# Kernel tuning notes

Hardware: AMD Instinct MI355X
Metric: run time of the kernel (lower is better)

Reference implementation:

```python
import jax, jax.numpy as jnp
import numpy as np

C = 1024
HEADS = 8
HD = C // HEADS
SF = 2
EPS = 1e-6
N, D, H, W = 2, 32, 40, 32


def _ln(x, w, b):
    m = jnp.mean(x, -1, keepdims=True)
    v = jnp.mean((x - m) ** 2, -1, keepdims=True)
    return (x - m) * jax.lax.rsqrt(v + EPS) * w + b


def _mlp2(x, w1, b1, w2, b2):
    # Linear -> exact GELU -> Linear (matches nn.Sequential(Linear, GELU, Linear))
    return jax.nn.gelu(x @ w1.T + b1, approximate=False) @ w2.T + b2


def setup_inputs() -> dict:
    key = jax.random.key(0)
    ks = jax.random.split(key, 24)
    p = lambda i, shape: jax.random.normal(ks[i], shape, jnp.float32) * 0.02
    return {
        "x": jax.random.normal(ks[0], (N, D, H, W, C), jnp.float32),
        "q_w": p(1, (C, C)),
        "k_w1": p(2, (C, C)), "k_b1": p(3, (C,)),
        "k_w2": p(4, (C, C)), "k_b2": p(5, (C,)),
        "v_w1": p(6, (C, C)), "v_b1": p(7, (C,)),
        "v_w2": p(8, (C, C)), "v_b2": p(9, (C,)),
        "lnq_w": jnp.ones((C,), jnp.float32), "lnq_b": jnp.zeros((C,), jnp.float32),
        "lnk_w": jnp.ones((C,), jnp.float32), "lnk_b": jnp.zeros((C,), jnp.float32),
        "lnv_w": jnp.ones((C,), jnp.float32), "lnv_b": jnp.zeros((C,), jnp.float32),
        "in_w": p(10, (3 * C, C)), "in_b": p(11, (3 * C,)),
        "out_w": p(12, (C, C)), "out_b": p(13, (C,)),
        "mlp_w1": p(14, (2 * C, C)), "mlp_b1": p(15, (2 * C,)),
        "mlp_w2": p(16, (2 * C, 2 * C)), "mlp_b2": p(17, (2 * C,)),
    }


def reference(x, q_w, k_w1, k_b1, k_w2, k_b2, v_w1, v_b1, v_w2, v_b2,
              lnq_w, lnq_b, lnk_w, lnk_b, lnv_w, lnv_b,
              in_w, in_b, out_w, out_b, mlp_w1, mlp_b1, mlp_w2, mlp_b2):
    n, d, h, w, c = x.shape
    dg, hg, wg = d // SF, h // SF, w // SF
    cube = SF ** 3

    x_flat = x.reshape(n, -1, c)                      # [N, T, C], T = D*H*W
    k = _ln(_mlp2(x_flat, k_w1, k_b1, k_w2, k_b2), lnk_w, lnk_b)
    v = _ln(_mlp2(x_flat, v_w1, v_b1, v_w2, v_b2), lnv_w, lnv_b)

    # Trilinear downsample by exactly 2 (align_corners=False) == 2x2x2 mean pool.
    q = x.reshape(n, dg, SF, hg, SF, wg, SF, c).mean(axis=(2, 4, 6))
    q = q.reshape(n, -1, c)                            # [N, Q, C]
    query = _ln(q @ q_w.T, lnq_w, lnq_b)               # q_proj_1 has no bias

    def regions(t):
        t = t.reshape(n, dg, SF, hg, SF, wg, SF, c)
        t = t.transpose(0, 1, 3, 5, 2, 4, 6, 7)
        return t.reshape(n, dg * hg * wg, cube, c)     # [N, Q, 8, C]

    k_r = regions(k)
    v_r = regions(v)

    wq, wk, wv = in_w[:C], in_w[C:2 * C], in_w[2 * C:]
    bq, bk, bv = in_b[:C], in_b[C:2 * C], in_b[2 * C:]
    qh = (query @ wq.T + bq).reshape(n, -1, HEADS, HD)           # [N,Q,h,hd]
    kh = (k_r @ wk.T + bk).reshape(n, -1, cube, HEADS, HD)       # [N,Q,8,h,hd]
    vh = (v_r @ wv.T + bv).reshape(n, -1, cube, HEADS, HD)

    scale = 1.0 / np.sqrt(HD).astype(np.float32)
    scores = jnp.einsum('nqhd,nqkhd->nqhk', qh, kh) * scale
    attn = jax.nn.softmax(scores, axis=-1)
    o = jnp.einsum('nqhk,nqkhd->nqhd', attn, vh).reshape(n, -1, c)
    o = o @ out_w.T + out_b                            # MHA out_proj

    o = _mlp2(o, mlp_w1, mlp_b1, mlp_w2, mlp_b2)       # [N, Q, 2C]
    return o.reshape(n, dg, hg, wg, 2 * c)
```

## Files before the change

kernel.cpp:

```cpp
#include <hip/hip_runtime.h>

typedef __attribute__((ext_vector_type(8))) short bf16x8;
typedef __attribute__((ext_vector_type(4))) float f32x4;
typedef unsigned short u16;

__device__ inline u16 f2b(float f) {
  union { float f; unsigned u; } x; x.f = f;
  unsigned r = x.u + 0x7FFFu + ((x.u >> 16) & 1u);
  return (u16)(r >> 16);
}
__device__ inline float b2f(u16 s) {
  union { unsigned u; float f; } x; x.u = ((unsigned)s) << 16;
  return x.f;
}
__device__ inline float gelu_f(float v) {
  return 0.5f * v * (1.0f + erff(v * 0.70710678118654752f));
}
__device__ inline void gll16(const void* g, void* lds) {
  __builtin_amdgcn_global_load_lds((const __attribute__((address_space(1))) void*)g,
                                   (__attribute__((address_space(3))) void*)lds,
                                   16, 0, 0);
}

__global__ __launch_bounds__(256) void cvt_w(const float* __restrict__ s,
                                             u16* __restrict__ d, int n4) {
  int i = blockIdx.x * 256 + threadIdx.x;
  if (i < n4) {
    float4 v = ((const float4*)s)[i];
    ushort4 o; o.x = f2b(v.x); o.y = f2b(v.y); o.z = f2b(v.z); o.w = f2b(v.w);
    ((ushort4*)d)[i] = o;
  }
}

__global__ __launch_bounds__(256) void cat_bias(const float* __restrict__ a,
                                                const float* __restrict__ b,
                                                float* __restrict__ o) {
  int i = blockIdx.x * 256 + threadIdx.x;
  if (i < 1024) { o[i] = a[i]; o[1024 + i] = b[i]; }
}

__global__ __launch_bounds__(256) void pool_cvt(const float* __restrict__ xg,
                                                u16* __restrict__ Xb,
                                                u16* __restrict__ Qp) {
  int qr = blockIdx.x;
  int wgi = qr & 15;
  int hgi = (qr >> 4) % 20;
  int dgi = qr / 320;
  int c = threadIdx.x * 4;
  float sx = 0.f, sy = 0.f, sz = 0.f, sw = 0.f;
#pragma unroll
  for (int j = 0; j < 8; ++j) {
    int tr = ((2 * dgi + (j >> 2)) * 40 + (2 * hgi + ((j >> 1) & 1))) * 32 +
             (2 * wgi + (j & 1));
    long off = (long)tr * 1024 + c;
    float4 v = *(const float4*)&xg[off];
    ushort4 o; o.x = f2b(v.x); o.y = f2b(v.y); o.z = f2b(v.z); o.w = f2b(v.w);
    *(ushort4*)&Xb[off] = o;
    sx += v.x; sy += v.y; sz += v.z; sw += v.w;
  }
  ushort4 o;
  o.x = f2b(sx * 0.125f); o.y = f2b(sy * 0.125f);
  o.z = f2b(sz * 0.125f); o.w = f2b(sw * 0.125f);
  *(ushort4*)&Qp[(long)qr * 1024 + c] = o;
}

__global__ __launch_bounds__(256) void ln_ip(u16* __restrict__ X,
                                             const float* __restrict__ w,
                                             const float* __restrict__ b) {
  long row = blockIdx.x;
  int c = threadIdx.x * 4;
  ushort4 v = *(const ushort4*)&X[row * 1024 + c];
  float f0 = b2f(v.x), f1 = b2f(v.y), f2 = b2f(v.z), f3 = b2f(v.w);
  float s = f0 + f1 + f2 + f3;
  float q = f0 * f0 + f1 * f1 + f2 * f2 + f3 * f3;
#pragma unroll
  for (int off = 32; off >= 1; off >>= 1) {
    s += __shfl_xor(s, off);
    q += __shfl_xor(q, off);
  }
  __shared__ float red[8];
  int wv = threadIdx.x >> 6, ln = threadIdx.x & 63;
  if (ln == 0) { red[wv] = s; red[4 + wv] = q; }
  __syncthreads();
  s = red[0] + red[1] + red[2] + red[3];
  q = red[4] + red[5] + red[6] + red[7];
  float mean = s * (1.f / 1024.f);
  float var = q * (1.f / 1024.f) - mean * mean;
  float rs = rsqrtf(var + 1e-6f);
  float4 wv4 = *(const float4*)&w[c];
  float4 bv4 = *(const float4*)&b[c];
  ushort4 o;
  o.x = f2b((f0 - mean) * rs * wv4.x + bv4.x);
  o.y = f2b((f1 - mean) * rs * wv4.y + bv4.y);
  o.z = f2b((f2 - mean) * rs * wv4.z + bv4.z);
  o.w = f2b((f3 - mean) * rs * wv4.w + bv4.w);
  *(ushort4*)&X[row * 1024 + c] = o;
}

#define BK 32
template <int EPI>
__global__ __launch_bounds__(256) void gemm_bt(const u16* __restrict__ A,
                                               const u16* __restrict__ B,
                                               const float* __restrict__ bias,
                                               float* __restrict__ Cf,
                                               u16* __restrict__ Cb,
                                               int M, int N, int K, int lda,
                                               int nbx, int nby) {
  __shared__ __align__(16) u16 As0[128 * BK];
  __shared__ __align__(16) u16 Bs0[128 * BK];
  __shared__ __align__(16) u16 As1[128 * BK];
  __shared__ __align__(16) u16 Bs1[128 * BK];
  const int tid = threadIdx.x;

  int L = blockIdx.x, bx, by;
  if ((nbx & 7) == 0) {
    int xcd = L & 7, j = L >> 3, ppx = nbx >> 3;
    int pj = j / nby;
    bx = xcd * ppx + pj;
    by = j - pj * nby;
  } else {
    bx = L % nbx;
    by = L / nbx;
  }
  const int bm = bx * 128, bn = by * 128;

  const int l = tid & 63, wv = tid >> 6;
  const int wm = (wv >> 1) * 64, wn = (wv & 1) * 64;
  const int lr = l & 15, kg = l >> 4;

  const int ea = tid * 8, eb = (256 + tid) * 8;
  const int ra = ea >> 5, ca = ea & 31;
  const int rb = eb >> 5, cbn = eb & 31;
  int gra = bm + ra; if (gra > M - 1) gra = M - 1;
  int grb = bm + rb; if (grb > M - 1) grb = M - 1;
  const u16* pa0 = A + (long)gra * lda + ca;
  const u16* pa1 = A + (long)grb * lda + cbn;
  const u16* pb0 = B + (long)(bn + ra) * K + ca;
  const u16* pb1 = B + (long)(bn + rb) * K + cbn;

  f32x4 acc[4][4] = {};
  const int nt = K / BK;

#define STAGE(AS, BS, k0)                \
  do {                                   \
    gll16(pa0 + (k0), &(AS)[ea]);        \
    gll16(pb0 + (k0), &(BS)[ea]);        \
    gll16(pa1 + (k0), &(AS)[eb]);        \
    gll16(pb1 + (k0), &(BS)[eb]);        \
  } while (0)

#define COMPUTE(AS, BS)                                                       \
  do {                                                                        \
    bf16x8 af[4], bfr[4];                                                     \
    _Pragma("unroll") for (int m = 0; m < 4; ++m)                             \
        af[m] = *(const bf16x8*)&(AS)[(wm + m * 16 + lr) * BK + kg * 8];      \
    _Pragma("unroll") for (int n = 0; n < 4; ++n)                             \
        bfr[n] = *(const bf16x8*)&(BS)[(wn + n * 16 + lr) * BK + kg * 8];     \
    _Pragma("unroll") for (int m = 0; m < 4; ++m)                             \
        _Pragma("unroll") for (int n = 0; n < 4; ++n)                         \
            acc[m][n] = __builtin_amdgcn_mfma_f32_16x16x32_bf16(              \
                af[m], bfr[n], acc[m][n], 0, 0, 0);                           \
  } while (0)

  STAGE(As0, Bs0, 0);
  __syncthreads();
  for (int t = 0; t < nt; t += 2) {
    if (t + 1 < nt) STAGE(As1, Bs1, (t + 1) * BK);
    COMPUTE(As0, Bs0);
    __syncthreads();
    if (t + 2 < nt) STAGE(As0, Bs0, (t + 2) * BK);
    COMPUTE(As1, Bs1);
    __syncthreads();
  }
#undef STAGE
#undef COMPUTE

#pragma unroll
  for (int m = 0; m < 4; ++m) {
    int row0 = bm + wm + m * 16 + kg * 4;
#pragma unroll
    for (int n = 0; n < 4; ++n) {
      int col = bn + wn + n * 16 + lr;
      float bsv = (EPI == 3) ? 0.f : bias[col];
#pragma unroll
      for (int r = 0; r < 4; ++r) {
        int row = row0 + r;
        if (row < M) {
          float v = acc[m][n][r] + bsv;
          if (EPI == 1) v = gelu_f(v);
          if (EPI == 2) Cf[(long)row * N + col] = v;
          else Cb[(long)row * N + col] = f2b(v);
        }
      }
    }
  }
}

__global__ __launch_bounds__(256) void attn_k(const u16* __restrict__ QH,
                                              const u16* __restrict__ KH,
                                              const u16* __restrict__ VH,
                                              u16* __restrict__ O) {
  int qr = blockIdx.x;
  int wgi = qr & 15;
  int hgi = (qr >> 4) % 20;
  int dgi = qr / 320;
  int c0 = (threadIdx.x >> 5) * 128 + (threadIdx.x & 31) * 4;
  ushort4 qv = *(const ushort4*)&QH[(long)qr * 1024 + c0];
  float q0 = b2f(qv.x), q1 = b2f(qv.y), q2 = b2f(qv.z), q3 = b2f(qv.w);
  long trs[8];
  float sc[8];
#pragma unroll
  for (int j = 0; j < 8; ++j) {
    int tr = ((2 * dgi + (j >> 2)) * 40 + (2 * hgi + ((j >> 1) & 1))) * 32 +
             (2 * wgi + (j & 1));
    trs[j] = (long)tr * 1024 + c0;
    ushort4 kv = *(const ushort4*)&KH[trs[j]];
    float p = q0 * b2f(kv.x) + q1 * b2f(kv.y) + q2 * b2f(kv.z) + q3 * b2f(kv.w);
    p += __shfl_xor(p, 16); p += __shfl_xor(p, 8); p += __shfl_xor(p, 4);
    p += __shfl_xor(p, 2);  p += __shfl_xor(p, 1);
    sc[j] = p * 0.088388347648318447f;
  }
  float mx = sc[0];
#pragma unroll
  for (int j = 1; j < 8; ++j) mx = fmaxf(mx, sc[j]);
  float ssum = 0.f;
#pragma unroll
  for (int j = 0; j < 8; ++j) { sc[j] = expf(sc[j] - mx); ssum += sc[j]; }
  float inv = 1.0f / ssum;
  float o0 = 0, o1 = 0, o2 = 0, o3 = 0;
#pragma unroll
  for (int j = 0; j < 8; ++j) {
    ushort4 vv = *(const ushort4*)&VH[trs[j]];
    float p = sc[j] * inv;
    o0 += p * b2f(vv.x); o1 += p * b2f(vv.y);
    o2 += p * b2f(vv.z); o3 += p * b2f(vv.w);
  }
  ushort4 ov; ov.x = f2b(o0); ov.y = f2b(o1); ov.z = f2b(o2); ov.w = f2b(o3);
  *(ushort4*)&O[(long)qr * 1024 + c0] = ov;
}

extern "C" void kernel_launch(void* const* d_in, const int* in_sizes, int n_in,
                              void* d_out, int out_size, void* d_ws,
                              size_t ws_size, hipStream_t stream) {
  const float* x      = (const float*)d_in[0];
  const float* q_w    = (const float*)d_in[1];
  const float* k_w1   = (const float*)d_in[2];
  const float* k_b1   = (const float*)d_in[3];
  const float* k_w2   = (const float*)d_in[4];
  const float* k_b2   = (const float*)d_in[5];
  const float* v_w1   = (const float*)d_in[6];
  const float* v_b1   = (const float*)d_in[7];
  const float* v_w2   = (const float*)d_in[8];
  const float* v_b2   = (const float*)d_in[9];
  const float* lnq_w  = (const float*)d_in[10];
  const float* lnq_b  = (const float*)d_in[11];
  const float* lnk_w  = (const float*)d_in[12];
  const float* lnk_b  = (const float*)d_in[13];
  const float* lnv_w  = (const float*)d_in[14];
  const float* lnv_b  = (const float*)d_in[15];
  const float* in_w   = (const float*)d_in[16];
  const float* in_b   = (const float*)d_in[17];
  const float* out_w  = (const float*)d_in[18];
  const float* out_b  = (const float*)d_in[19];
  const float* mlp_w1 = (const float*)d_in[20];
  const float* mlp_b1 = (const float*)d_in[21];
  const float* mlp_w2 = (const float*)d_in[22];
  const float* mlp_b2 = (const float*)d_in[23];
  float* out = (float*)d_out;

  char* base = (char*)d_ws;
  size_t off = 0;
  auto alloc_us = [&](size_t elems) -> u16* {
    u16* r = (u16*)(base + off);
    off += ((elems * 2 + 255) & ~(size_t)255);
    return r;
  };
  const size_t CC = 1024 * 1024;
  u16* wb_q   = alloc_us(CC);
  u16* wb_kv1 = alloc_us(2 * CC);
  u16* wb_k2  = alloc_us(CC);
  u16* wb_v2  = alloc_us(CC);
  u16* wb_in  = alloc_us(3 * CC);
  u16* wb_out = alloc_us(CC);
  u16* wb_m1  = alloc_us(2 * CC);
  u16* wb_m2  = alloc_us(4 * CC);
  float* b_kv1 = (float*)(base + off); off += 2048 * 4;

  auto cvt = [&](const float* s, u16* d, size_t n) {
    int n4 = (int)(n / 4);
    cvt_w<<<(n4 + 255) / 256, 256, 0, stream>>>(s, d, n4);
  };
  cvt(q_w, wb_q, CC);
  cvt(k_w1, wb_kv1, CC);        cvt(v_w1, wb_kv1 + CC, CC);
  cvt(k_w2, wb_k2, CC);         cvt(v_w2, wb_v2, CC);
  cvt(in_w, wb_in, 3 * CC);     cvt(out_w, wb_out, CC);
  cvt(mlp_w1, wb_m1, 2 * CC);   cvt(mlp_w2, wb_m2, 4 * CC);
  cat_bias<<<4, 256, 0, stream>>>(k_b1, v_b1, b_kv1);

  int s = 16;
  for (int cand = 1; cand <= 16; cand <<= 1) {
    size_t Tc_ = 40960ull / cand;
    size_t need = off + Tc_ * 11520ull + (1ull << 20);
    if (need <= ws_size) { s = cand; break; }
  }
  const int dcount = 32 / s;
  const int dgc = dcount / 2;
  const int Tc = dcount * 1280;
  const int Tq = dgc * 320;

  u16* Xb  = alloc_us((size_t)Tc * 1024);
  u16* Hb2 = alloc_us((size_t)Tc * 2048);
  u16* Kb  = alloc_us((size_t)Tc * 1024);
  u16* Vb  = alloc_us((size_t)Tc * 1024);
  u16* Qp  = alloc_us((size_t)Tq * 1024);
  u16* QQ  = alloc_us((size_t)Tq * 1024);
  u16* QHb = alloc_us((size_t)Tq * 1024);
  u16* Ob  = alloc_us((size_t)Tq * 1024);
  u16* O2  = alloc_us((size_t)Tq * 1024);
  u16* Hm  = Kb;

  auto launch_gemm = [&](int EPI, const u16* A, const u16* B, const float* bias,
                         float* Cf, u16* Cb, int M, int N, int K, int lda) {
    int nbx = (M + 127) / 128, nby = N / 128;
    dim3 g(nbx * nby);
    switch (EPI) {
      case 0: gemm_bt<0><<<g, 256, 0, stream>>>(A, B, bias, Cf, Cb, M, N, K, lda, nbx, nby); break;
      case 1: gemm_bt<1><<<g, 256, 0, stream>>>(A, B, bias, Cf, Cb, M, N, K, lda, nbx, nby); break;
      case 2: gemm_bt<2><<<g, 256, 0, stream>>>(A, B, bias, Cf, Cb, M, N, K, lda, nbx, nby); break;
      default: gemm_bt<3><<<g, 256, 0, stream>>>(A, B, bias, Cf, Cb, M, N, K, lda, nbx, nby); break;
    }
  };

  for (int n = 0; n < 2; ++n) {
    for (int sl = 0; sl < s; ++sl) {
      long tok0 = (long)n * 40960 + (long)sl * dcount * 1280;
      long q0g  = (long)n * 5120 + (long)sl * dgc * 320;
      const float* xg = x + tok0 * 1024;

      pool_cvt<<<Tq, 256, 0, stream>>>(xg, Xb, Qp);

      launch_gemm(1, Xb, wb_kv1, b_kv1, nullptr, Hb2, Tc, 2048, 1024, 1024);
      launch_gemm(0, Hb2, wb_k2, k_b2, nullptr, Kb, Tc, 1024, 1024, 2048);
      ln_ip<<<Tc, 256, 0, stream>>>(Kb, lnk_w, lnk_b);
      launch_gemm(0, Hb2 + 1024, wb_v2, v_b2, nullptr, Vb, Tc, 1024, 1024, 2048);
      ln_ip<<<Tc, 256, 0, stream>>>(Vb, lnv_w, lnv_b);

      launch_gemm(3, Qp, wb_q, nullptr, nullptr, QQ, Tq, 1024, 1024, 1024);
      ln_ip<<<Tq, 256, 0, stream>>>(QQ, lnq_w, lnq_b);
      launch_gemm(0, QQ, wb_in, in_b, nullptr, QHb, Tq, 1024, 1024, 1024);

      launch_gemm(0, Kb, wb_in + CC, in_b + 1024, nullptr, Xb, Tc, 1024, 1024, 1024);
      launch_gemm(0, Vb, wb_in + 2 * CC, in_b + 2048, nullptr, Hb2, Tc, 1024, 1024, 1024);

      attn_k<<<Tq, 256, 0, stream>>>(QHb, Xb, Hb2, Ob);

      launch_gemm(0, Ob, wb_out, out_b, nullptr, O2, Tq, 1024, 1024, 1024);
      launch_gemm(1, O2, wb_m1, mlp_b1, nullptr, Hm, Tq, 2048, 1024, 1024);
      launch_gemm(2, Hm, wb_m2, mlp_b2, out + q0g * 2048, nullptr, Tq, 2048, 2048, 2048);
    }
  }
}
```

Measured before the change: 2.314 ms.

## Replace 128x128 GEMM with 256x256 tile, 8-wave, swizzled LDS pipelined kernel

Replaces the 128x128x32 double-buffered GEMM with a 256x256x64 kernel that runs 8 waves per block and uses 128 KB of dynamic LDS. LDS rows are XOR-swizzled to avoid bank conflicts, and global-to-LDS loads are split into half-tiles interleaved between four MFMA phases. Those phases use s_setprio and explicit vmcnt waits to overlap memory with compute. The goal is more operand reuse per tile and less load latency. The cost is fewer blocks in flight, wasted work on partial tiles, and heavy register pressure from a 32-accumulator tile per wave.

```diff
diff --git a/kernel.cpp b/kernel.cpp
--- a/kernel.cpp
+++ b/kernel.cpp
@@ -97,20 +97,25 @@
   *(ushort4*)&X[row * 1024 + c] = o;
 }
 
-#define BK 32
+#define HALF 8192
+#define MFMA16(a, b, c) __builtin_amdgcn_mfma_f32_16x16x32_bf16((a), (b), (c), 0, 0, 0)
+
 template <int EPI>
-__global__ __launch_bounds__(256) void gemm_bt(const u16* __restrict__ A,
-                                               const u16* __restrict__ B,
-                                               const float* __restrict__ bias,
-                                               float* __restrict__ Cf,
-                                               u16* __restrict__ Cb,
-                                               int M, int N, int K, int lda,
-                                               int nbx, int nby) {
-  __shared__ __align__(16) u16 As0[128 * BK];
-  __shared__ __align__(16) u16 Bs0[128 * BK];
-  __shared__ __align__(16) u16 As1[128 * BK];
-  __shared__ __align__(16) u16 Bs1[128 * BK];
+__global__ __launch_bounds__(512, 2) void gemm256(const u16* __restrict__ A,
+                                                  const u16* __restrict__ B,
+                                                  const float* __restrict__ bias,
+                                                  float* __restrict__ Cf,
+                                                  u16* __restrict__ Cb,
+                                                  int M, int N, int K, int lda,
+                                                  int nbx, int nby) {
+  extern __shared__ u16 lds[];
+  u16* ASm = lds;
+  u16* BSm = lds + 4 * HALF;
   const int tid = threadIdx.x;
+  const int l = tid & 63, w = tid >> 6;
+  const int wr = w >> 2, wc = w & 3;
+  const int lr = l & 15, kg = l >> 4;
+  const int e7 = l & 7;
 
   int L = blockIdx.x, bx, by;
   if ((nbx & 7) == 0) {
@@ -122,74 +127,145 @@
     bx = L % nbx;
     by = L / nbx;
   }
-  const int bm = bx * 128, bn = by * 128;
-
-  const int l = tid & 63, wv = tid >> 6;
-  const int wm = (wv >> 1) * 64, wn = (wv & 1) * 64;
-  const int lr = l & 15, kg = l >> 4;
-
-  const int ea = tid * 8, eb = (256 + tid) * 8;
-  const int ra = ea >> 5, ca = ea & 31;
-  const int rb = eb >> 5, cbn = eb & 31;
-  int gra = bm + ra; if (gra > M - 1) gra = M - 1;
-  int grb = bm + rb; if (grb > M - 1) grb = M - 1;
-  const u16* pa0 = A + (long)gra * lda + ca;
-  const u16* pa1 = A + (long)grb * lda + cbn;
-  const u16* pb0 = B + (long)(bn + ra) * K + ca;
-  const u16* pb1 = B + (long)(bn + rb) * K + cbn;
-
-  f32x4 acc[4][4] = {};
-  const int nt = K / BK;
-
-#define STAGE(AS, BS, k0)                \
-  do {                                   \
-    gll16(pa0 + (k0), &(AS)[ea]);        \
-    gll16(pb0 + (k0), &(BS)[ea]);        \
-    gll16(pa1 + (k0), &(AS)[eb]);        \
-    gll16(pb1 + (k0), &(BS)[eb]);        \
-  } while (0)
-
-#define COMPUTE(AS, BS)                                                       \
-  do {                                                                        \
-    bf16x8 af[4], bfr[4];                                                     \
-    _Pragma("unroll") for (int m = 0; m < 4; ++m)                             \
-        af[m] = *(const bf16x8*)&(AS)[(wm + m * 16 + lr) * BK + kg * 8];      \
-    _Pragma("unroll") for (int n = 0; n < 4; ++n)                             \
-        bfr[n] = *(const bf16x8*)&(BS)[(wn + n * 16 + lr) * BK + kg * 8];     \
-    _Pragma("unroll") for (int m = 0; m < 4; ++m)                             \
-        _Pragma("unroll") for (int n = 0; n < 4; ++n)                         \
-            acc[m][n] = __builtin_amdgcn_mfma_f32_16x16x32_bf16(              \
-                af[m], bfr[n], acc[m][n], 0, 0, 0);                           \
-  } while (0)
-
-  STAGE(As0, Bs0, 0);
-  __syncthreads();
-  for (int t = 0; t < nt; t += 2) {
-    if (t + 1 < nt) STAGE(As1, Bs1, (t + 1) * BK);
-    COMPUTE(As0, Bs0);
-    __syncthreads();
-    if (t + 2 < nt) STAGE(As0, Bs0, (t + 2) * BK);
-    COMPUTE(As1, Bs1);
-    __syncthreads();
-  }
-#undef STAGE
-#undef COMPUTE
-
-#pragma unroll
-  for (int m = 0; m < 4; ++m) {
-    int row0 = bm + wm + m * 16 + kg * 4;
+  const int bm = bx * 256, bn = by * 256;
+
+  const int c0 = w * 64 + l, c1 = 512 + c0;
+  const int r0 = c0 >> 3, cs0 = (c0 & 7) ^ (r0 & 7);
+  const int r1 = c1 >> 3, cs1 = (c1 & 7) ^ (r1 & 7);
+  const u16* Ab = A + (long)bm * lda;
+  const u16* Bb = B + (long)bn * K;
+  int a0r0 = min(bm + r0, M - 1) - bm;
+  int a0r1 = min(bm + r1, M - 1) - bm;
+  int a1r0 = min(bm + 128 + r0, M - 1) - bm;
+  int a1r1 = min(bm + 128 + r1, M - 1) - bm;
+  const int oA00 = a0r0 * lda + cs0 * 8, oA01 = a0r1 * lda + cs1 * 8;
+  const int oA10 = a1r0 * lda + cs0 * 8, oA11 = a1r1 * lda + cs1 * 8;
+  const int oB00 = r0 * K + cs0 * 8, oB01 = r1 * K + cs1 * 8;
+  const int oB10 = (128 + r0) * K + cs0 * 8, oB11 = (128 + r1) * K + cs1 * 8;
+  const int d0 = c0 * 8, d1 = c1 * 8;
+
+  const int sw0 = ((kg) ^ e7) * 8;
+  const int sw1 = ((4 + kg) ^ e7) * 8;
+
+  f32x4 acc[8][4] = {};
+  bf16x8 af[4][2], bf[2][2][2];
+  const int nt = K / 64;
+
+#define STG_A(slot, o0_, o1_, ko) do { \
+    gll16(Ab + (o0_) + (ko), ASm + (slot) * HALF + d0); \
+    gll16(Ab + (o1_) + (ko), ASm + (slot) * HALF + d1); } while (0)
+#define STG_B(slot, o0_, o1_, ko) do { \
+    gll16(Bb + (o0_) + (ko), BSm + (slot) * HALF + d0); \
+    gll16(Bb + (o1_) + (ko), BSm + (slot) * HALF + d1); } while (0)
+
+  STG_A(0, oA00, oA01, 0); STG_A(1, oA10, oA11, 0);
+  STG_B(0, oB00, oB01, 0); STG_B(1, oB10, oB11, 0);
+  STG_A(2, oA00, oA01, 64); STG_B(2, oB00, oB01, 64); STG_B(3, oB10, oB11, 64);
+  asm volatile("s_waitcnt vmcnt(6)" ::: "memory");
+  __builtin_amdgcn_s_barrier();
+
+  const int rbA = wr * 64 + lr;
+  const int rbB = (wc & 1) * 64 + lr;
+
+  for (int t = 0; t < nt; ++t) {
+    const int p = t & 1, qp = p ^ 1;
+    const int kn1 = (t + 1 < nt ? t + 1 : nt - 1) * 64;
+    const int kn2 = (t + 2 < nt ? t + 2 : nt - 1) * 64;
+    const u16* sa0 = ASm + (p * 2 + 0) * HALF;
+    const u16* sa1 = ASm + (p * 2 + 1) * HALF;
+    const u16* sb = BSm + (p * 2 + (wc >> 1)) * HALF;
+
+#pragma unroll
+    for (int mq = 0; mq < 4; ++mq) {
+      af[mq][0] = *(const bf16x8*)&sa0[(rbA + mq * 16) * 64 + sw0];
+      af[mq][1] = *(const bf16x8*)&sa0[(rbA + mq * 16) * 64 + sw1];
+    }
+#pragma unroll
+    for (int nn = 0; nn < 2; ++nn) {
+      bf[0][nn][0] = *(const bf16x8*)&sb[(rbB + nn * 16) * 64 + sw0];
+      bf[0][nn][1] = *(const bf16x8*)&sb[(rbB + nn * 16) * 64 + sw1];
+    }
+    STG_A(qp * 2 + 1, oA10, oA11, kn1);
+    __builtin_amdgcn_s_barrier();
+    __builtin_amdgcn_s_setprio(1);
+#pragma unroll
+    for (int mq = 0; mq < 4; ++mq)
+#pragma unroll
+      for (int nn = 0; nn < 2; ++nn) {
+        acc[mq][nn] = MFMA16(af[mq][0], bf[0][nn][0], acc[mq][nn]);
+        acc[mq][nn] = MFMA16(af[mq][1], bf[0][nn][1], acc[mq][nn]);
+      }
+    __builtin_amdgcn_s_setprio(0);
+    __builtin_amdgcn_s_barrier();
+
+#pragma unroll
+    for (int nn = 0; nn < 2; ++nn) {
+      bf[1][nn][0] = *(const bf16x8*)&sb[(rbB + (2 + nn) * 16) * 64 + sw0];
+      bf[1][nn][1] = *(const bf16x8*)&sb[(rbB + (2 + nn) * 16) * 64 + sw1];
+    }
+    STG_A(p * 2 + 0, oA00, oA01, kn2);
+    __builtin_amdgcn_s_barrier();
+    __builtin_amdgcn_s_setprio(1);
+#pragma unroll
+    for (int mq = 0; mq < 4; ++mq)
+#pragma unroll
+      for (int nn = 0; nn < 2; ++nn) {
+        acc[mq][2 + nn] = MFMA16(af[mq][0], bf[1][nn][0], acc[mq][2 + nn]);
+        acc[mq][2 + nn] = MFMA16(af[mq][1], bf[1][nn][1], acc[mq][2 + nn]);
+      }
+    __builtin_amdgcn_s_setprio(0);
+    __builtin_amdgcn_s_barrier();
+
+#pragma unroll
+    for (int mq = 0; mq < 4; ++mq) {
+      af[mq][0] = *(const bf16x8*)&sa1[(rbA + mq * 16) * 64 + sw0];
+      af[mq][1] = *(const bf16x8*)&sa1[(rbA + mq * 16) * 64 + sw1];
+    }
+    STG_B(p * 2 + 0, oB00, oB01, kn2);
+    __builtin_amdgcn_s_barrier();
+    __builtin_amdgcn_s_setprio(1);
+#pragma unroll
+    for (int mq = 0; mq < 4; ++mq)
+#pragma unroll
+      for (int nn = 0; nn < 2; ++nn) {
+        acc[4 + mq][nn] = MFMA16(af[mq][0], bf[0][nn][0], acc[4 + mq][nn]);
+        acc[4 + mq][nn] = MFMA16(af[mq][1], bf[0][nn][1], acc[4 + mq][nn]);
+      }
+    __builtin_amdgcn_s_setprio(0);
+    __builtin_amdgcn_s_barrier();
+
+    STG_B(p * 2 + 1, oB10, oB11, kn2);
+    asm volatile("s_waitcnt vmcnt(6)" ::: "memory");
+    __builtin_amdgcn_s_barrier();
+    __builtin_amdgcn_s_setprio(1);
+#pragma unroll
+    for (int mq = 0; mq < 4; ++mq)
+#pragma unroll
+      for (int nn = 0; nn < 2; ++nn) {
+        acc[4 + mq][2 + nn] = MFMA16(af[mq][0], bf[1][nn][0], acc[4 + mq][2 + nn]);
+        acc[4 + mq][2 + nn] = MFMA16(af[mq][1], bf[1][nn][1], acc[4 + mq][2 + nn]);
+      }
+    __builtin_amdgcn_s_setprio(0);
+    __builtin_amdgcn_s_barrier();
+  }
+  asm volatile("s_waitcnt vmcnt(0)" ::: "memory");
+#undef STG_A
+#undef STG_B
+
+#pragma unroll
+  for (int m = 0; m < 8; ++m) {
+    int row = bm + (m >> 2) * 128 + wr * 64 + (m & 3) * 16 + kg * 4;
 #pragma unroll
     for (int n = 0; n < 4; ++n) {
-      int col = bn + wn + n * 16 + lr;
+      int col = bn + wc * 64 + n * 16 + lr;
       float bsv = (EPI == 3) ? 0.f : bias[col];
 #pragma unroll
       for (int r = 0; r < 4; ++r) {
-        int row = row0 + r;
-        if (row < M) {
+        if (row + r < M) {
           float v = acc[m][n][r] + bsv;
           if (EPI == 1) v = gelu_f(v);
-          if (EPI == 2) Cf[(long)row * N + col] = v;
-          else Cb[(long)row * N + col] = f2b(v);
+          if (EPI == 2) Cf[(long)(row + r) * N + col] = v;
+          else Cb[(long)(row + r) * N + col] = f2b(v);
         }
       }
     }
@@ -268,6 +344,11 @@
   const float* mlp_b2 = (const float*)d_in[23];
   float* out = (float*)d_out;
 
+  hipFuncSetAttribute((const void*)gemm256<0>, hipFuncAttributeMaxDynamicSharedMemorySize, 131072);
+  hipFuncSetAttribute((const void*)gemm256<1>, hipFuncAttributeMaxDynamicSharedMemorySize, 131072);
+  hipFuncSetAttribute((const void*)gemm256<2>, hipFuncAttributeMaxDynamicSharedMemorySize, 131072);
+  hipFuncSetAttribute((const void*)gemm256<3>, hipFuncAttributeMaxDynamicSharedMemorySize, 131072);
+
   char* base = (char*)d_ws;
   size_t off = 0;
   auto alloc_us = [&](size_t elems) -> u16* {
@@ -321,13 +402,13 @@
 
   auto launch_gemm = [&](int EPI, const u16* A, const u16* B, const float* bias,
                          float* Cf, u16* Cb, int M, int N, int K, int lda) {
-    int nbx = (M + 127) / 128, nby = N / 128;
+    int nbx = (M + 255) / 256, nby = N / 256;
     dim3 g(nbx * nby);
     switch (EPI) {
-      case 0: gemm_bt<0><<<g, 256, 0, stream>>>(A, B, bias, Cf, Cb, M, N, K, lda, nbx, nby); break;
-      case 1: gemm_bt<1><<<g, 256, 0, stream>>>(A, B, bias, Cf, Cb, M, N, K, lda, nbx, nby); break;
-      case 2: gemm_bt<2><<<g, 256, 0, stream>>>(A, B, bias, Cf, Cb, M, N, K, lda, nbx, nby); break;
-      default: gemm_bt<3><<<g, 256, 0, stream>>>(A, B, bias, Cf, Cb, M, N, K, lda, nbx, nby); break;
+      case 0: gemm256<0><<<g, 512, 131072, stream>>>(A, B, bias, Cf, Cb, M, N, K, lda, nbx, nby); break;
+      case 1: gemm256<1><<<g, 512, 131072, stream>>>(A, B, bias, Cf, Cb, M, N, K, lda, nbx, nby); break;
+      case 2: gemm256<2><<<g, 512, 131072, stream>>>(A, B, bias, Cf, Cb, M, N, K, lda, nbx, nby); break;
+      default: gemm256<3><<<g, 512, 131072, stream>>>(A, B, bias, Cf, Cb, M, N, K, lda, nbx, nby); break;
     }
   };
 
```

Result: slower. 2.685 ms (+16.0%).

## Replace LDS-staged GEMM with direct global-to-register fragment loads

Applied to the files above, without the earlier changes.

The GEMM no longer stages A and B tiles through shared memory with async global-to-LDS copies. Each wave now loads its MFMA fragments straight from global memory into registers with a two-deep register double buffer, and all block barriers are removed. This is meant to cut LDS round trips and synchronisation, and a launch-bounds occupancy hint is added. The cost is duplicated global/L2 reads between waves that share rows or columns, and less coalesced access.

```diff
diff --git a/kernel.cpp b/kernel.cpp
--- a/kernel.cpp
+++ b/kernel.cpp
@@ -15,11 +15,6 @@
 }
 __device__ inline float gelu_f(float v) {
   return 0.5f * v * (1.0f + erff(v * 0.70710678118654752f));
-}
-__device__ inline void gll16(const void* g, void* lds) {
-  __builtin_amdgcn_global_load_lds((const __attribute__((address_space(1))) void*)g,
-                                   (__attribute__((address_space(3))) void*)lds,
-                                   16, 0, 0);
 }
 
 __global__ __launch_bounds__(256) void cvt_w(const float* __restrict__ s,
@@ -97,21 +92,16 @@
   *(ushort4*)&X[row * 1024 + c] = o;
 }
 
-#define BK 32
+#define MFMA16(a, b, c) __builtin_amdgcn_mfma_f32_16x16x32_bf16((a), (b), (c), 0, 0, 0)
+
 template <int EPI>
-__global__ __launch_bounds__(256) void gemm_bt(const u16* __restrict__ A,
-                                               const u16* __restrict__ B,
-                                               const float* __restrict__ bias,
-                                               float* __restrict__ Cf,
-                                               u16* __restrict__ Cb,
-                                               int M, int N, int K, int lda,
-                                               int nbx, int nby) {
-  __shared__ __align__(16) u16 As0[128 * BK];
-  __shared__ __align__(16) u16 Bs0[128 * BK];
-  __shared__ __align__(16) u16 As1[128 * BK];
-  __shared__ __align__(16) u16 Bs1[128 * BK];
-  const int tid = threadIdx.x;
-
+__global__ __launch_bounds__(256, 3) void gemm_rd(const u16* __restrict__ A,
+                                                  const u16* __restrict__ B,
+                                                  const float* __restrict__ bias,
+                                                  float* __restrict__ Cf,
+                                                  u16* __restrict__ Cb,
+                                                  int M, int N, int K, int lda,
+                                                  int nbx, int nby) {
   int L = blockIdx.x, bx, by;
   if ((nbx & 7) == 0) {
     int xcd = L & 7, j = L >> 3, ppx = nbx >> 3;
@@ -124,56 +114,58 @@
   }
   const int bm = bx * 128, bn = by * 128;
 
-  const int l = tid & 63, wv = tid >> 6;
+  const int l = threadIdx.x & 63, wv = threadIdx.x >> 6;
   const int wm = (wv >> 1) * 64, wn = (wv & 1) * 64;
   const int lr = l & 15, kg = l >> 4;
 
-  const int ea = tid * 8, eb = (256 + tid) * 8;
-  const int ra = ea >> 5, ca = ea & 31;
-  const int rb = eb >> 5, cbn = eb & 31;
-  int gra = bm + ra; if (gra > M - 1) gra = M - 1;
-  int grb = bm + rb; if (grb > M - 1) grb = M - 1;
-  const u16* pa0 = A + (long)gra * lda + ca;
-  const u16* pa1 = A + (long)grb * lda + cbn;
-  const u16* pb0 = B + (long)(bn + ra) * K + ca;
-  const u16* pb1 = B + (long)(bn + rb) * K + cbn;
+  const u16* pa[4];
+  const u16* pb[4];
+#pragma unroll
+  for (int m = 0; m < 4; ++m) {
+    int row = bm + wm + m * 16 + lr;
+    if (row > M - 1) row = M - 1;
+    pa[m] = A + (long)row * lda + kg * 8;
+  }
+#pragma unroll
+  for (int n = 0; n < 4; ++n)
+    pb[n] = B + (long)(bn + wn + n * 16 + lr) * K + kg * 8;
 
   f32x4 acc[4][4] = {};
-  const int nt = K / BK;
-
-#define STAGE(AS, BS, k0)                \
-  do {                                   \
-    gll16(pa0 + (k0), &(AS)[ea]);        \
-    gll16(pb0 + (k0), &(BS)[ea]);        \
-    gll16(pa1 + (k0), &(AS)[eb]);        \
-    gll16(pb1 + (k0), &(BS)[eb]);        \
-  } while (0)
-
-#define COMPUTE(AS, BS)                                                       \
-  do {                                                                        \
-    bf16x8 af[4], bfr[4];                                                     \
-    _Pragma("unroll") for (int m = 0; m < 4; ++m)                             \
-        af[m] = *(const bf16x8*)&(AS)[(wm + m * 16 + lr) * BK + kg * 8];      \
-    _Pragma("unroll") for (int n = 0; n < 4; ++n)                             \
-        bfr[n] = *(const bf16x8*)&(BS)[(wn + n * 16 + lr) * BK + kg * 8];     \
-    _Pragma("unroll") for (int m = 0; m < 4; ++m)                             \
-        _Pragma("unroll") for (int n = 0; n < 4; ++n)                         \
-            acc[m][n] = __builtin_amdgcn_mfma_f32_16x16x32_bf16(              \
-                af[m], bfr[n], acc[m][n], 0, 0, 0);                           \
-  } while (0)
-
-  STAGE(As0, Bs0, 0);
-  __syncthreads();
+  bf16x8 a0[4], b0[4], a1[4], b1[4];
+
+#pragma unroll
+  for (int m = 0; m < 4; ++m) a0[m] = *(const bf16x8*)(pa[m]);
+#pragma unroll
+  for (int n = 0; n < 4; ++n) b0[n] = *(const bf16x8*)(pb[n]);
+
+  const int nt = K / 32;
   for (int t = 0; t < nt; t += 2) {
-    if (t + 1 < nt) STAGE(As1, Bs1, (t + 1) * BK);
-    COMPUTE(As0, Bs0);
-    __syncthreads();
-    if (t + 2 < nt) STAGE(As0, Bs0, (t + 2) * BK);
-    COMPUTE(As1, Bs1);
-    __syncthreads();
-  }
-#undef STAGE
-#undef COMPUTE
+    const int k1 = (t + 1) * 32, k2 = (t + 2) * 32;
+    if (t + 1 < nt) {
+#pragma unroll
+      for (int m = 0; m < 4; ++m) a1[m] = *(const bf16x8*)(pa[m] + k1);
+#pragma unroll
+      for (int n = 0; n < 4; ++n) b1[n] = *(const bf16x8*)(pb[n] + k1);
+    }
+#pragma unroll
+    for (int m = 0; m < 4; ++m)
+#pragma unroll
+      for (int n = 0; n < 4; ++n)
+        acc[m][n] = MFMA16(a0[m], b0[n], acc[m][n]);
+    if (t + 2 < nt) {
+#pragma unroll
+      for (int m = 0; m < 4; ++m) a0[m] = *(const bf16x8*)(pa[m] + k2);
+#pragma unroll
+      for (int n = 0; n < 4; ++n) b0[n] = *(const bf16x8*)(pb[n] + k2);
+    }
+    if (t + 1 < nt) {
+#pragma unroll
+      for (int m = 0; m < 4; ++m)
+#pragma unroll
+        for (int n = 0; n < 4; ++n)
+          acc[m][n] = MFMA16(a1[m], b1[n], acc[m][n]);
+    }
+  }
 
 #pragma unroll
   for (int m = 0; m < 4; ++m) {
@@ -324,10 +316,10 @@
     int nbx = (M + 127) / 128, nby = N / 128;
     dim3 g(nbx * nby);
     switch (EPI) {
-      case 0: gemm_bt<0><<<g, 256, 0, stream>>>(A, B, bias, Cf, Cb, M, N, K, lda, nbx, nby); break;
-      case 1: gemm_bt<1><<<g, 256, 0, stream>>>(A, B, bias, Cf, Cb, M, N, K, lda, nbx, nby); break;
-      case 2: gemm_bt<2><<<g, 256, 0, stream>>>(A, B, bias, Cf, Cb, M, N, K, lda, nbx, nby); break;
-      default: gemm_bt<3><<<g, 256, 0, stream>>>(A, B, bias, Cf, Cb, M, N, K, lda, nbx, nby); break;
+      case 0: gemm_rd<0><<<g, 256, 0, stream>>>(A, B, bias, Cf, Cb, M, N, K, lda, nbx, nby); break;
+      case 1: gemm_rd<1><<<g, 256, 0, stream>>>(A, B, bias, Cf, Cb, M, N, K, lda, nbx, nby); break;
+      case 2: gemm_rd<2><<<g, 256, 0, stream>>>(A, B, bias, Cf, Cb, M, N, K, lda, nbx, nby); break;
+      default: gemm_rd<3><<<g, 256, 0, stream>>>(A, B, bias, Cf, Cb, M, N, K, lda, nbx, nby); break;
     }
   };
 
```

Result: slower. 4.856 ms (+109.8%).

## Add 256x256-tile GEMM kernel with swizzled LDS for large projections

Applied to the files above, without the earlier changes.

Adds a second GEMM kernel that uses 512-thread blocks, a 256x256 output tile, a K step of 64 and double-buffered XOR-swizzled LDS loaded through global_load_lds, backed by 128KB of dynamic shared memory. The launcher sends large GEMMs (at least 256 of the big tiles) to this kernel and keeps the old 128x128 kernel for the smaller ones. The goal is more arithmetic per byte loaded and fewer LDS bank conflicts on the dominant token-wise MLP GEMMs. The cost is lower occupancy because of the large LDS footprint, and worse tile quantization on the edges of the grid.

```diff
diff --git a/kernel.cpp b/kernel.cpp
--- a/kernel.cpp
+++ b/kernel.cpp
@@ -97,6 +97,8 @@
   *(ushort4*)&X[row * 1024 + c] = o;
 }
 
+#define MFMA16(a, b, c) __builtin_amdgcn_mfma_f32_16x16x32_bf16((a), (b), (c), 0, 0, 0)
+
 #define BK 32
 template <int EPI>
 __global__ __launch_bounds__(256) void gemm_bt(const u16* __restrict__ A,
@@ -158,8 +160,7 @@
         bfr[n] = *(const bf16x8*)&(BS)[(wn + n * 16 + lr) * BK + kg * 8];     \
     _Pragma("unroll") for (int m = 0; m < 4; ++m)                             \
         _Pragma("unroll") for (int n = 0; n < 4; ++n)                         \
-            acc[m][n] = __builtin_amdgcn_mfma_f32_16x16x32_bf16(              \
-                af[m], bfr[n], acc[m][n], 0, 0, 0);                           \
+            acc[m][n] = MFMA16(af[m], bfr[n], acc[m][n]);                     \
   } while (0)
 
   STAGE(As0, Bs0, 0);
@@ -190,6 +191,133 @@
           if (EPI == 1) v = gelu_f(v);
           if (EPI == 2) Cf[(long)row * N + col] = v;
           else Cb[(long)row * N + col] = f2b(v);
+        }
+      }
+    }
+  }
+}
+
+template <int EPI>
+__global__ __launch_bounds__(512, 2) void g256(const u16* __restrict__ A,
+                                               const u16* __restrict__ B,
+                                               const float* __restrict__ bias,
+                                               float* __restrict__ Cf,
+                                               u16* __restrict__ Cb,
+                                               int M, int N, int K, int lda,
+                                               int nbx, int nby) {
+  extern __shared__ u16 lds[];
+  const int tid = threadIdx.x;
+  const int l = tid & 63, w = tid >> 6;
+  const int wr = w >> 2, wc = w & 3;
+  const int lr = l & 15, kg = l >> 4;
+
+  int L = blockIdx.x, bx, by;
+  if ((nbx & 7) == 0) {
+    int xcd = L & 7, j = L >> 3, ppx = nbx >> 3;
+    int pj = j / nby;
+    bx = xcd * ppx + pj;
+    by = j - pj * nby;
+  } else {
+    bx = L % nbx;
+    by = L / nbx;
+  }
+  const int bm = bx * 256, bn = by * 256;
+
+  const int c0 = w * 64 + l, c1 = 512 + c0;
+  const int r0 = c0 >> 3, cs0 = (c0 & 7) ^ (r0 & 7);
+  const int r1 = c1 >> 3, cs1 = (c1 & 7) ^ (r1 & 7);
+  const u16* Ab = A + (long)bm * lda;
+  const u16* Bb = B + (long)bn * K;
+  int a0r0 = min(bm + r0, M - 1) - bm;
+  int a0r1 = min(bm + r1, M - 1) - bm;
+  int a1r0 = min(bm + 128 + r0, M - 1) - bm;
+  int a1r1 = min(bm + 128 + r1, M - 1) - bm;
+  const int oA00 = a0r0 * lda + cs0 * 8, oA01 = a0r1 * lda + cs1 * 8;
+  const int oA10 = a1r0 * lda + cs0 * 8, oA11 = a1r1 * lda + cs1 * 8;
+  const int oB00 = r0 * K + cs0 * 8, oB01 = r1 * K + cs1 * 8;
+  const int oB10 = (128 + r0) * K + cs0 * 8, oB11 = (128 + r1) * K + cs1 * 8;
+  const int d0 = c0 * 8, d1 = c1 * 8;
+
+  const int sw0 = ((kg) ^ (l & 7)) * 8;
+  const int sw1 = ((4 + kg) ^ (l & 7)) * 8;
+
+  const int rA = wr * 64 + lr;
+  const int rB = (wc & 1) * 64 + lr;
+  const int bhalf = (wc >> 1) * 8192;
+
+  f32x4 acc[8][4] = {};
+  const int nt = K / 64;
+
+#define STG(P, ko)                                                   \
+  do {                                                               \
+    u16* ap = lds + (P) * 32768;                                     \
+    u16* bp = lds + 16384 + (P) * 32768;                             \
+    gll16(Ab + oA00 + (ko), ap + d0);                                \
+    gll16(Ab + oA01 + (ko), ap + d1);                                \
+    gll16(Ab + oA10 + (ko), ap + 8192 + d0);                         \
+    gll16(Ab + oA11 + (ko), ap + 8192 + d1);                         \
+    gll16(Bb + oB00 + (ko), bp + d0);                                \
+    gll16(Bb + oB01 + (ko), bp + d1);                                \
+    gll16(Bb + oB10 + (ko), bp + 8192 + d0);                         \
+    gll16(Bb + oB11 + (ko), bp + 8192 + d1);                         \
+  } while (0)
+
+#define CMP(P)                                                                 \
+  do {                                                                         \
+    const u16* ap = lds + (P) * 32768;                                         \
+    const u16* bp = lds + 16384 + (P) * 32768 + bhalf;                         \
+    bf16x8 af[4][2], bfr[4][2];                                                \
+    _Pragma("unroll") for (int nn = 0; nn < 4; ++nn) {                         \
+      bfr[nn][0] = *(const bf16x8*)&bp[(rB + nn * 16) * 64 + sw0];             \
+      bfr[nn][1] = *(const bf16x8*)&bp[(rB + nn * 16) * 64 + sw1];             \
+    }                                                                          \
+    _Pragma("unroll") for (int mq = 0; mq < 4; ++mq) {                         \
+      af[mq][0] = *(const bf16x8*)&ap[(rA + mq * 16) * 64 + sw0];              \
+      af[mq][1] = *(const bf16x8*)&ap[(rA + mq * 16) * 64 + sw1];              \
+    }                                                                          \
+    _Pragma("unroll") for (int mq = 0; mq < 4; ++mq)                           \
+      _Pragma("unroll") for (int nn = 0; nn < 4; ++nn) {                       \
+        acc[mq][nn] = MFMA16(af[mq][0], bfr[nn][0], acc[mq][nn]);              \
+        acc[mq][nn] = MFMA16(af[mq][1], bfr[nn][1], acc[mq][nn]);              \
+      }                                                                        \
+    _Pragma("unroll") for (int mq = 0; mq < 4; ++mq) {                         \
+      af[mq][0] = *(const bf16x8*)&ap[8192 + (rA + mq * 16) * 64 + sw0];       \
+      af[mq][1] = *(const bf16x8*)&ap[8192 + (rA + mq * 16) * 64 + sw1];       \
+    }                                                                          \
+    _Pragma("unroll") for (int mq = 0; mq < 4; ++mq)                           \
+      _Pragma("unroll") for (int nn = 0; nn < 4; ++nn) {                       \
+        acc[4 + mq][nn] = MFMA16(af[mq][0], bfr[nn][0], acc[4 + mq][nn]);      \
+        acc[4 + mq][nn] = MFMA16(af[mq][1], bfr[nn][1], acc[4 + mq][nn]);      \
+      }                                                                        \
+  } while (0)
+
+  STG(0, 0);
+  __syncthreads();
+  for (int t = 0; t < nt; t += 2) {
+    if (t + 1 < nt) STG(1, (t + 1) * 64);
+    CMP(0);
+    __syncthreads();
+    if (t + 2 < nt) STG(0, (t + 2) * 64);
+    CMP(1);
+    __syncthreads();
+  }
+#undef STG
+#undef CMP
+
+#pragma unroll
+  for (int m = 0; m < 8; ++m) {
+    int row = bm + (m >> 2) * 128 + wr * 64 + (m & 3) * 16 + kg * 4;
+#pragma unroll
+    for (int n = 0; n < 4; ++n) {
+      int col = bn + wc * 64 + n * 16 + lr;
+      float bsv = (EPI == 3) ? 0.f : bias[col];
+#pragma unroll
+      for (int r = 0; r < 4; ++r) {
+        if (row + r < M) {
+          float v = acc[m][n][r] + bsv;
+          if (EPI == 1) v = gelu_f(v);
+          if (EPI == 2) Cf[(long)(row + r) * N + col] = v;
+          else Cb[(long)(row + r) * N + col] = f2b(v);
         }
       }
     }
@@ -268,6 +396,11 @@
   const float* mlp_b2 = (const float*)d_in[23];
   float* out = (float*)d_out;
 
+  hipFuncSetAttribute((const void*)g256<0>, hipFuncAttributeMaxDynamicSharedMemorySize, 131072);
+  hipFuncSetAttribute((const void*)g256<1>, hipFuncAttributeMaxDynamicSharedMemorySize, 131072);
+  hipFuncSetAttribute((const void*)g256<2>, hipFuncAttributeMaxDynamicSharedMemorySize, 131072);
+  hipFuncSetAttribute((const void*)g256<3>, hipFuncAttributeMaxDynamicSharedMemorySize, 131072);
+
   char* base = (char*)d_ws;
   size_t off = 0;
   auto alloc_us = [&](size_t elems) -> u16* {
@@ -321,13 +454,25 @@
 
   auto launch_gemm = [&](int EPI, const u16* A, const u16* B, const float* bias,
                          float* Cf, u16* Cb, int M, int N, int K, int lda) {
-    int nbx = (M + 127) / 128, nby = N / 128;
-    dim3 g(nbx * nby);
-    switch (EPI) {
-      case 0: gemm_bt<0><<<g, 256, 0, stream>>>(A, B, bias, Cf, Cb, M, N, K, lda, nbx, nby); break;
-      case 1: gemm_bt<1><<<g, 256, 0, stream>>>(A, B, bias, Cf, Cb, M, N, K, lda, nbx, nby); break;
-      case 2: gemm_bt<2><<<g, 256, 0, stream>>>(A, B, bias, Cf, Cb, M, N, K, lda, nbx, nby); break;
-      default: gemm_bt<3><<<g, 256, 0, stream>>>(A, B, bias, Cf, Cb, M, N, K, lda, nbx, nby); break;
+    int b256 = (M / 256) * (N / 256);
+    if ((M % 128) == 0 && (N % 256) == 0 && b256 >= 256) {
+      int nbx = (M + 255) / 256, nby = N / 256;
+      dim3 g(nbx * nby);
+      switch (EPI) {
+        case 0: g256<0><<<g, 512, 131072, stream>>>(A, B, bias, Cf, Cb, M, N, K, lda, nbx, nby); break;
+        case 1: g256<1><<<g, 512, 131072, stream>>>(A, B, bias, Cf, Cb, M, N, K, lda, nbx, nby); break;
+        case 2: g256<2><<<g, 512, 131072, stream>>>(A, B, bias, Cf, Cb, M, N, K, lda, nbx, nby); break;
+        default: g256<3><<<g, 512, 131072, stream>>>(A, B, bias, Cf, Cb, M, N, K, lda, nbx, nby); break;
+      }
+    } else {
+      int nbx = (M + 127) / 128, nby = N / 128;
+      dim3 g(nbx * nby);
+      switch (EPI) {
+        case 0: gemm_bt<0><<<g, 256, 0, stream>>>(A, B, bias, Cf, Cb, M, N, K, lda, nbx, nby); break;
+        case 1: gemm_bt<1><<<g, 256, 0, stream>>>(A, B, bias, Cf, Cb, M, N, K, lda, nbx, nby); break;
+        case 2: gemm_bt<2><<<g, 256, 0, stream>>>(A, B, bias, Cf, Cb, M, N, K, lda, nbx, nby); break;
+        default: gemm_bt<3><<<g, 256, 0, stream>>>(A, B, bias, Cf, Cb, M, N, K, lda, nbx, nby); break;
+      }
     }
   };
 
```

Measured after the change: 2.461 ms. +6.3%, slower.
